# Performance work log

Hardware: AMD Instinct MI355X
Metric: run time of the kernel (lower is better)

## Reference

```python
import jax, jax.numpy as jnp
import numpy as np
from jax import lax

D = 8          # conv_out_size
HID = 128      # lstm hidden
EMB = 32       # word embed
GD = 256       # g/f mlp width


def _coords():
    # faithful to cvt_coord with python3 float division on first component
    c = np.zeros((D * D, 2), dtype=np.float32)
    for i in range(D * D):
        c[i, 0] = (i / D - D / 2) / (D / 2.0)
        c[i, 1] = (i % D - D / 2) / (D / 2.0)
    return jnp.asarray(c)


def _conv_bn(x, k, b, gamma, beta):
    y = lax.conv_general_dilated(x, k, (2, 2), [(1, 1), (1, 1)],
                                 dimension_numbers=('NCHW', 'OIHW', 'NCHW'))
    y = jax.nn.relu(y + b[None, :, None, None])
    m = y.mean((0, 2, 3))
    v = ((y - m[None, :, None, None]) ** 2).mean((0, 2, 3))  # biased var (train-mode BN)
    y = (y - m[None, :, None, None]) * lax.rsqrt(v + 1e-5)[None, :, None, None]
    return gamma[None, :, None, None] * y + beta[None, :, None, None]


def setup_inputs() -> dict:
    key = jax.random.key(0)
    ks = iter(jax.random.split(key, 48))
    B, T, QV, AV = 64, 18, 90, 28
    n = lambda sh, s=0.1: jax.random.normal(next(ks), sh, jnp.float32) * s
    inp = {
        'img': jax.random.normal(next(ks), (B, 3, 128, 128), jnp.float32),
        'qst_idxs': jax.random.randint(next(ks), (B, T), 0, QV),
        'emb': n((QV, EMB)).at[0].set(0.0),  # padding_idx=0
        'W_ih': n((4 * HID, EMB)), 'W_hh': n((4 * HID, HID)),
        'b_ih': n((4 * HID,)), 'b_hh': n((4 * HID,)),
        'k1': n((24, 3, 3, 3)), 'cb1': n((24,)), 'g1': jnp.ones((24,)), 'be1': jnp.zeros((24,)),
        'k2': n((24, 24, 3, 3)), 'cb2': n((24,)), 'g2': jnp.ones((24,)), 'be2': jnp.zeros((24,)),
        'k3': n((24, 24, 3, 3)), 'cb3': n((24,)), 'g3': jnp.ones((24,)), 'be3': jnp.zeros((24,)),
        'k4': n((24, 24, 3, 3)), 'cb4': n((24,)), 'g4': jnp.ones((24,)), 'be4': jnp.zeros((24,)),
        'Wg1': n((GD, 180)), 'bg1': n((GD,)),
        'Wg2': n((GD, GD)), 'bg2': n((GD,)),
        'Wg3': n((GD, GD)), 'bg3': n((GD,)),
        'Wg4': n((GD, GD)), 'bg4': n((GD,)),
        'Wf1': n((GD, GD)), 'bf1': n((GD,)),
        'Wf2': n((GD, GD)), 'bf2': n((GD,)),
        'Wf3': n((AV, GD)), 'bf3': n((AV,)),
        'h0': jax.random.normal(next(ks), (B, HID), jnp.float32),
        'c0': jax.random.normal(next(ks), (B, HID), jnp.float32),
    }
    return inp


def reference(img, qst_idxs, emb, W_ih, W_hh, b_ih, b_hh,
              k1, cb1, g1, be1, k2, cb2, g2, be2, k3, cb3, g3, be3, k4, cb4, g4, be4,
              Wg1, bg1, Wg2, bg2, Wg3, bg3, Wg4, bg4,
              Wf1, bf1, Wf2, bf2, Wf3, bf3, h0, c0):
    B = img.shape[0]
    # --- question encoder: embedding (padding_idx=0) + LSTM, take final CELL state ---
    we = emb[qst_idxs] * (qst_idxs != 0)[..., None].astype(emb.dtype)  # [B,T,32]

    def step(carry, x_t):
        h, c = carry
        gates = x_t @ W_ih.T + h @ W_hh.T + (b_ih + b_hh)
        i, f, g, o = jnp.split(gates, 4, axis=-1)
        c = jax.nn.sigmoid(f) * c + jax.nn.sigmoid(i) * jnp.tanh(g)
        h = jax.nn.sigmoid(o) * jnp.tanh(c)
        return (h, c), None

    (h_n, c_n), _ = lax.scan(step, (h0, c0), we.transpose(1, 0, 2))
    qst = c_n  # original uses self.hidden[1][-1] == cell state, [B,128]

    # --- conv stack ---
    x = _conv_bn(img, k1, cb1, g1, be1)
    x = _conv_bn(x, k2, cb2, g2, be2)
    x = _conv_bn(x, k3, cb3, g3, be3)
    x = _conv_bn(x, k4, cb4, g4, be4)  # [B,24,8,8]

    xf = x.reshape(B, 24, D * D).transpose(0, 2, 1)            # [B,64,24]
    xf = jnp.concatenate([xf, jnp.broadcast_to(_coords(), (B, D * D, 2))], 2)  # [B,64,26]

    # --- g-MLP over all pairs; first linear decomposed across x_i / x_j / qst ---
    # pair (k,j) feature = [x_flat[j](26), x_flat[k](26), qst(128)]
    Ai = xf @ Wg1[:, :26].T                    # [B,64,256], x_i part (index j)
    Aj = xf @ Wg1[:, 26:52].T                  # [B,64,256], x_j part (index k)
    Q = qst @ Wg1[:, 52:].T + bg1              # [B,256]
    h = jax.nn.relu(Ai[:, None, :, :] + Aj[:, :, None, :] + Q[:, None, None, :])  # [B,64,64,256]
    h = jax.nn.relu(h @ Wg2.T + bg2)
    h = jax.nn.relu(h @ Wg3.T + bg3)
    h = jax.nn.relu(h @ Wg4.T + bg4)
    xg = h.sum((1, 2))                          # [B,256] sum-pool over pairs

    # --- f-MLP (dropout = identity in eval) ---
    xfc = jax.nn.relu(xg @ Wf1.T + bf1)
    xfc = jax.nn.relu(xfc @ Wf2.T + bf2)
    logits = xfc @ Wf3.T + bf3
    return jax.nn.log_softmax(logits, axis=-1)
```

## Files before the change

kernel.cpp:

```cpp
#include <hip/hip_runtime.h>
#include <math.h>

typedef __bf16 bf16x8 __attribute__((ext_vector_type(8)));
typedef float  f32x16 __attribute__((ext_vector_type(16)));

#define DEVFN __device__ __forceinline__

DEVFN unsigned short f2bfh(float f) {
    __bf16 h = (__bf16)f;
    union { __bf16 h; unsigned short u; } v; v.h = h;
    return v.u;
}
DEVFN float sigmoidf_(float x) { return 1.0f / (1.0f + expf(-x)); }

__global__ void cvt_kernel(const float* __restrict__ Wg2, const float* __restrict__ Wg3,
                           const float* __restrict__ Wg4,
                           const float* __restrict__ Wih, const float* __restrict__ Whh,
                           unsigned short* __restrict__ Wt2, unsigned short* __restrict__ Wt3,
                           unsigned short* __restrict__ Wt4,
                           float* __restrict__ WihT, float* __restrict__ WhhT)
{
    int i = blockIdx.x * 512 + threadIdx.x;
    if (i < 196608) {
        int seg = i >> 16, idx = i & 65535;
        const float* src = (seg == 0) ? Wg2 : (seg == 1) ? Wg3 : Wg4;
        unsigned short* dst = (seg == 0) ? Wt2 : (seg == 1) ? Wt3 : Wt4;
        int col = idx >> 8, k = idx & 255;
        dst[(k >> 3)*2048 + col*8 + (k & 7)] = f2bfh(src[idx]);
    } else {
        int j = i - 196608;
        if (j < 65536) {
            int d = j >> 9, row = j & 511;
            WhhT[j] = Whh[row*128 + d];
        } else if (j < 81920) {
            j -= 65536;
            int d = j >> 9, row = j & 511;
            WihT[j] = Wih[row*32 + d];
        }
    }
}

__global__ void lstm_kernel(const int* __restrict__ qidx, const float* __restrict__ emb,
                            const float* __restrict__ WihT, const float* __restrict__ WhhT,
                            const float* __restrict__ bih, const float* __restrict__ bhh,
                            const float* __restrict__ h0, const float* __restrict__ c0,
                            float* __restrict__ qst)
{
    int b = blockIdx.x, tid = threadIdx.x;
    __shared__ float hs[128], cs[128], xs[32], gs[512];
    if (tid < 128) { hs[tid] = h0[b*128 + tid]; cs[tid] = c0[b*128 + tid]; }
    float bsum = bih[tid] + bhh[tid];
    for (int t = 0; t < 18; ++t) {
        if (tid < 32) {
            int id = qidx[b*18 + t];
            xs[tid] = (id != 0) ? emb[id*32 + tid] : 0.0f;
        }
        __syncthreads();
        float g = bsum;
        #pragma unroll
        for (int d = 0; d < 32; ++d) g += xs[d] * WihT[d*512 + tid];
        #pragma unroll 8
        for (int d = 0; d < 128; ++d) g += hs[d] * WhhT[d*512 + tid];
        gs[tid] = g;
        __syncthreads();
        if (tid < 128) {
            float ig = sigmoidf_(gs[tid]);
            float fg = sigmoidf_(gs[128 + tid]);
            float gg = tanhf(gs[256 + tid]);
            float og = sigmoidf_(gs[384 + tid]);
            float cn = fg * cs[tid] + ig * gg;
            cs[tid] = cn;
            hs[tid] = og * tanhf(cn);
        }
        __syncthreads();
    }
    if (tid < 128) qst[b*128 + tid] = cs[tid];
}

__launch_bounds__(256, 4)
__global__ void conv1_kernel(const float* __restrict__ img, const float* __restrict__ wk,
                             const float* __restrict__ cb, float* __restrict__ y1)
{
    __shared__ float simg[3][9][128];
    __shared__ __align__(16) float wl[3][9][24];
    __shared__ float cbs[24];
    int b = blockIdx.x, t = blockIdx.y, tid = threadIdx.x;
    for (int i = tid; i < 648; i += 256) {
        int co = i / 27, rem = i % 27;
        wl[rem / 9][rem % 9][co] = wk[i];
    }
    if (tid < 24) cbs[tid] = cb[tid];
    int base = 8*t - 1;
    for (int i = tid; i < 3*9*128; i += 256) {
        int ci = i / (9*128); int r2 = i % (9*128);
        int row = r2 / 128, colx = r2 % 128;
        int ih = base + row;
        simg[ci][row][colx] = (ih >= 0 && ih < 128) ?
            img[((size_t)(b*3 + ci)*128 + ih)*128 + colx] : 0.f;
    }
    __syncthreads();

    int ow = tid & 63;
    int os = tid >> 6;
    int oh = t*4 + os;
    float* yb = y1 + ((size_t)b*24*64 + oh)*64 + ow;

    #pragma unroll
    for (int co4 = 0; co4 < 24; co4 += 4) {
        float a0 = 0.f, a1 = 0.f, a2 = 0.f, a3 = 0.f;
        #pragma unroll
        for (int ci = 0; ci < 3; ++ci)
          #pragma unroll
          for (int kh = 0; kh < 3; ++kh)
            #pragma unroll
            for (int kw = 0; kw < 3; ++kw) {
                int iw = ow*2 + kw - 1;
                float x = (iw >= 0 && iw < 128) ? simg[ci][2*os + kh][iw] : 0.f;
                float4 w4 = *reinterpret_cast<const float4*>(&wl[ci][kh*3 + kw][co4]);
                a0 += x*w4.x; a1 += x*w4.y; a2 += x*w4.z; a3 += x*w4.w;
            }
        yb[(size_t)(co4+0)*4096] = fmaxf(a0 + cbs[co4+0], 0.f);
        yb[(size_t)(co4+1)*4096] = fmaxf(a1 + cbs[co4+1], 0.f);
        yb[(size_t)(co4+2)*4096] = fmaxf(a2 + cbs[co4+2], 0.f);
        yb[(size_t)(co4+3)*4096] = fmaxf(a3 + cbs[co4+3], 0.f);
    }
}

__global__ void bn_partial_kernel(const float* __restrict__ y, float* __restrict__ part,
                                  int HW, int nb)
{
    int c = blockIdx.x;
    int s = blockIdx.y;
    int S = gridDim.y;
    int tid = threadIdx.x;
    int n4 = HW >> 2;
    float sum = 0.f, sum2 = 0.f;
    for (int b = s * nb; b < (s + 1) * nb; ++b) {
        const float4* p = reinterpret_cast<const float4*>(y + ((size_t)(b*24 + c)) * HW);
        for (int i = tid; i < n4; i += 256) {
            float4 v = p[i];
            sum  += v.x + v.y + v.z + v.w;
            sum2 += v.x*v.x + v.y*v.y + v.z*v.z + v.w*v.w;
        }
    }
    __shared__ float rs[256], rs2[256];
    rs[tid] = sum; rs2[tid] = sum2;
    __syncthreads();
    for (int st = 128; st > 0; st >>= 1) {
        if (tid < st) { rs[tid] += rs[tid + st]; rs2[tid] += rs2[tid + st]; }
        __syncthreads();
    }
    if (tid == 0) {
        part[(c * S + s) * 2]     = rs[0];
        part[(c * S + s) * 2 + 1] = rs2[0];
    }
}

#define BN_FOLD(bnp, gamma, beta, S, N, abs_, abo_, tid)                    \
    if (tid < 24) {                                                          \
        float s_ = 0.f, s2_ = 0.f;                                           \
        for (int i_ = 0; i_ < (S); ++i_) {                                   \
            s_  += (bnp)[((tid)*(S) + i_)*2];                                \
            s2_ += (bnp)[((tid)*(S) + i_)*2 + 1];                            \
        }                                                                    \
        float m_ = s_ / (N);                                                 \
        float v_ = s2_ / (N) - m_*m_;                                        \
        float r_ = rsqrtf(v_ + 1e-5f);                                       \
        float a_ = (gamma)[tid] * r_;                                        \
        (abs_)[tid] = a_; (abo_)[tid] = (beta)[tid] - m_*a_;                 \
    }

__launch_bounds__(128, 4)
__global__ void conv2_kernel(const float* __restrict__ y1, const float* __restrict__ wk,
                             const float* __restrict__ cb,
                             const float* __restrict__ bnp, const float* __restrict__ gamma,
                             const float* __restrict__ beta,
                             float* __restrict__ y2)
{
    __shared__ float sin2[24][5][64];
    __shared__ float wl[24][9][24];
    __shared__ float cbs[24];
    __shared__ float abs_[24], abo_[24];
    int b = blockIdx.x, t = blockIdx.y, tid = threadIdx.x;
    BN_FOLD(bnp, gamma, beta, 16, 262144, abs_, abo_, tid);
    for (int i = tid; i < 5184; i += 128) {
        int co = i / 216, rem = i % 216;
        int ci = rem / 9, tap = rem % 9;
        wl[ci][tap][co] = wk[i];
    }
    if (tid < 24) cbs[tid] = cb[tid];
    __syncthreads();
    int base = 4*t - 1;
    for (int i = tid; i < 24*5*64; i += 128) {
        int ci = i / (5*64); int r2 = i % (5*64);
        int row = r2 / 64, colx = r2 % 64;
        int ih = base + row;
        sin2[ci][row][colx] = (ih >= 0 && ih < 64) ?
            y1[((size_t)(b*24 + ci)*64 + ih)*64 + colx] * abs_[ci] + abo_[ci] : 0.f;
    }
    __syncthreads();

    int pos = tid & 63;
    int ow = pos & 31, os = pos >> 5;
    int ch = tid >> 6;
    int oh = 2*t + os;
    float acc[12];
    #pragma unroll
    for (int c = 0; c < 12; ++c) acc[c] = 0.f;

    for (int ci = 0; ci < 24; ++ci) {
        #pragma unroll
        for (int kh = 0; kh < 3; ++kh)
          #pragma unroll
          for (int kw = 0; kw < 3; ++kw) {
            int iw = ow*2 + kw - 1;
            float x = (iw >= 0 && iw < 64) ? sin2[ci][2*os + kh][iw] : 0.f;
            const float* wv = &wl[ci][kh*3 + kw][ch*12];
            #pragma unroll
            for (int c4 = 0; c4 < 3; ++c4) {
                float4 w4 = *reinterpret_cast<const float4*>(wv + c4*4);
                acc[c4*4+0] += x*w4.x;
                acc[c4*4+1] += x*w4.y;
                acc[c4*4+2] += x*w4.z;
                acc[c4*4+3] += x*w4.w;
            }
          }
    }
    #pragma unroll
    for (int c = 0; c < 12; ++c) {
        int co = ch*12 + c;
        y2[((size_t)(b*24 + co)*32 + oh)*32 + ow] = fmaxf(acc[c] + cbs[co], 0.f);
    }
}

__launch_bounds__(256, 2)
__global__ void conv_kernel(const float* __restrict__ in, const float* __restrict__ wk,
                            const float* __restrict__ cb,
                            const float* __restrict__ bnp, const float* __restrict__ gamma,
                            const float* __restrict__ beta, int S, int N,
                            float* __restrict__ out,
                            int Cin, int Hin, int Win, int Hout, int Wout)
{
    int cob = blockIdx.x;
    int co = cob % 24, b = cob / 24;
    int tid = threadIdx.x;
    __shared__ float sw[24*9];
    __shared__ float so9[9];
    __shared__ float bias;
    __shared__ float abs_[24], abo_[24];
    BN_FOLD(bnp, gamma, beta, S, N, abs_, abo_, tid);
    __syncthreads();
    if (tid < Cin*9) {
        int ci = tid / 9, t = tid % 9;
        sw[tid] = wk[(co*Cin + ci)*9 + t] * abs_[ci];
    }
    if (tid < 9) {
        float s = 0.f;
        for (int ci = 0; ci < Cin; ++ci)
            s += abo_[ci] * wk[(co*Cin + ci)*9 + tid];
        so9[tid] = s;
    }
    if (tid == 0) bias = cb[co];
    __syncthreads();

    int HW = Hout * Wout;
    int pos = tid;
    if (pos >= HW) return;
    int ow = pos % Wout, oh = pos / Wout;

    float acc = bias;
    #pragma unroll
    for (int kh = 0; kh < 3; ++kh) {
        int ih = oh*2 + kh - 1;
        bool vh = (ih >= 0 && ih < Hin);
        #pragma unroll
        for (int kw = 0; kw < 3; ++kw) {
            int iw = ow*2 + kw - 1;
            if (vh && iw >= 0 && iw < Win) acc += so9[kh*3 + kw];
        }
    }
    const float* ipb = in + ((size_t)b * Cin) * Hin * Win;
    for (int ci = 0; ci < Cin; ++ci) {
        const float* ip = ipb + (size_t)ci * Hin * Win;
        const float* swp = sw + ci*9;
        #pragma unroll
        for (int kh = 0; kh < 3; ++kh) {
            int ih = oh*2 + kh - 1;
            if (ih < 0 || ih >= Hin) continue;
            #pragma unroll
            for (int kw = 0; kw < 3; ++kw) {
                int iw = ow*2 + kw - 1;
                if (iw < 0 || iw >= Win) continue;
                acc += ip[ih*Win + iw] * swp[kh*3 + kw];
            }
        }
    }
    out[((size_t)(b*24 + co)) * HW + pos] = fmaxf(acc, 0.0f);
}

__global__ void aiajq_kernel(const float* __restrict__ y4,
                             const float* __restrict__ bnp, const float* __restrict__ gamma,
                             const float* __restrict__ beta,
                             const float* __restrict__ qst,
                             const float* __restrict__ Wg1, const float* __restrict__ bg1,
                             float* __restrict__ Ai, float* __restrict__ Aj, float* __restrict__ Q)
{
    int b = blockIdx.x, c = threadIdx.x;
    __shared__ float xfl[64 * 26];
    __shared__ float qv[128];
    __shared__ float abs_[24], abo_[24];
    BN_FOLD(bnp, gamma, beta, 1, 4096, abs_, abo_, c);
    __syncthreads();
    for (int i = c; i < 64*24; i += 256) {
        int p = i / 24, ch = i % 24;
        xfl[p*26 + ch] = y4[((size_t)(b*24 + ch)) * 64 + p] * abs_[ch] + abo_[ch];
    }
    if (c < 64) {
        xfl[c*26 + 24] = ((float)c / 8.0f - 4.0f) * 0.25f;
        xfl[c*26 + 25] = ((float)(c % 8) - 4.0f) * 0.25f;
    }
    if (c < 128) qv[c] = qst[b*128 + c];
    __syncthreads();
    const float* w = Wg1 + (size_t)c * 180;
    float wa[26], wb[26];
    #pragma unroll
    for (int d = 0; d < 26; ++d) { wa[d] = w[d]; wb[d] = w[26 + d]; }
    float q = bg1[c];
    for (int d = 0; d < 128; ++d) q += qv[d] * w[52 + d];
    Q[b*256 + c] = q;
    for (int j = 0; j < 64; ++j) {
        const float* xr = xfl + j*26;
        float sa = 0.f, sb = 0.f;
        #pragma unroll
        for (int d = 0; d < 26; ++d) { sa += xr[d]*wa[d]; sb += xr[d]*wb[d]; }
        Ai[((size_t)(b*64 + j))*256 + c] = sa;
        Aj[((size_t)(b*64 + j))*256 + c] = sb;
    }
}

__launch_bounds__(512, 4)
__global__ void gmlp_kernel(const float* __restrict__ Ai, const float* __restrict__ Aj,
                            const float* __restrict__ Q,
                            const unsigned short* __restrict__ Wt2, const float* __restrict__ bg2,
                            const unsigned short* __restrict__ Wt3, const float* __restrict__ bg3,
                            const unsigned short* __restrict__ Wt4, const float* __restrict__ bg4,
                            float* __restrict__ partial)
{
    constexpr int LDP = 264;
    __shared__ __align__(16) unsigned short buf[128 * LDP];
    int tid = threadIdx.x;
    int blk = blockIdx.x;
    int b = blk >> 5;
    int k0 = (blk & 31) << 1;

    {
        int g  = tid >> 8;
        int jh = (tid >> 7) & 1;
        int c2 = tid & 127;
        float2 aj = *((const float2*)(Aj + ((size_t)(b*64 + k0 + g))*256) + c2);
        float2 qq = *((const float2*)(Q + b*256) + c2);
        float a0 = aj.x + qq.x, a1 = aj.y + qq.y;
        const float2* aip = (const float2*)(Ai + ((size_t)b*64)*256) + c2;
        #pragma unroll 4
        for (int j = jh*32; j < jh*32 + 32; ++j) {
            float2 av = aip[(size_t)j*128];
            unsigned lo = f2bfh(fmaxf(av.x + a0, 0.f));
            unsigned hv = f2bfh(fmaxf(av.y + a1, 0.f));
            *(unsigned*)(&buf[(size_t)(g*64 + j)*LDP + 2*c2]) = lo | (hv << 16);
        }
    }
    __syncthreads();

    int l = tid & 63, w = tid >> 6;
    int rh = w >> 2;
    int cg = w & 3;
    int lid = l & 31, hi = l >> 5;
    int arow = rh*64 + lid;
    int colA = cg*64 + lid;
    int colB = colA + 32;

    const unsigned short* Ws[3] = {Wt2, Wt3, Wt4};
    const float* Bs[3] = {bg2, bg3, bg4};

    #pragma unroll
    for (int layer = 0; layer < 3; ++layer) {
        const unsigned short* W = Ws[layer];
        const float* bias = Bs[layer];
        f32x16 acc00, acc01, acc10, acc11;
        #pragma unroll
        for (int i = 0; i < 16; ++i) { acc00[i]=0.f; acc01[i]=0.f; acc10[i]=0.f; acc11[i]=0.f; }

        const unsigned short* wp0 = W + (size_t)hi*2048 + colA*8;
        const unsigned short* wp1 = W + (size_t)hi*2048 + colB*8;
        const unsigned short* ap  = buf + arow*LDP + hi*8;

        #pragma unroll
        for (int kk = 0; kk < 16; ++kk) {
            bf16x8 b0 = *reinterpret_cast<const bf16x8*>(wp0 + kk*4096);
            bf16x8 b1 = *reinterpret_cast<const bf16x8*>(wp1 + kk*4096);
            bf16x8 a0 = *reinterpret_cast<const bf16x8*>(ap + kk*16);
            bf16x8 a1 = *reinterpret_cast<const bf16x8*>(ap + 32*LDP + kk*16);
            acc00 = __builtin_amdgcn_mfma_f32_32x32x16_bf16(a0, b0, acc00, 0, 0, 0);
            acc01 = __builtin_amdgcn_mfma_f32_32x32x16_bf16(a0, b1, acc01, 0, 0, 0);
            acc10 = __builtin_amdgcn_mfma_f32_32x32x16_bf16(a1, b0, acc10, 0, 0, 0);
            acc11 = __builtin_amdgcn_mfma_f32_32x32x16_bf16(a1, b1, acc11, 0, 0, 0);
        }

        if (layer < 2) {
            float bc0 = bias[colA], bc1 = bias[colB];
            __syncthreads();
            #pragma unroll
            for (int reg = 0; reg < 16; ++reg) {
                int r0 = rh*64 + (reg & 3) + 8*(reg >> 2) + 4*hi;
                buf[r0*LDP + colA] = f2bfh(fmaxf(acc00[reg] + bc0, 0.f));
                buf[r0*LDP + colB] = f2bfh(fmaxf(acc01[reg] + bc1, 0.f));
                int r1 = r0 + 32;
                buf[r1*LDP + colA] = f2bfh(fmaxf(acc10[reg] + bc0, 0.f));
                buf[r1*LDP + colB] = f2bfh(fmaxf(acc11[reg] + bc1, 0.f));
            }
            __syncthreads();
        } else {
            float bc0 = bias[colA], bc1 = bias[colB];
            float cs0 = 0.f, cs1 = 0.f;
            #pragma unroll
            for (int reg = 0; reg < 16; ++reg) {
                cs0 += fmaxf(acc00[reg] + bc0, 0.f) + fmaxf(acc10[reg] + bc0, 0.f);
                cs1 += fmaxf(acc01[reg] + bc1, 0.f) + fmaxf(acc11[reg] + bc1, 0.f);
            }
            cs0 += __shfl_xor(cs0, 32);
            cs1 += __shfl_xor(cs1, 32);
            if (hi == 0) {
                float* pp = partial + ((size_t)blk*2 + rh)*256;
                pp[colA] = cs0;
                pp[colB] = cs1;
            }
        }
    }
}

__global__ void fmlp_kernel(const float* __restrict__ partial,
                            const float* __restrict__ Wf1, const float* __restrict__ bf1,
                            const float* __restrict__ Wf2, const float* __restrict__ bf2,
                            const float* __restrict__ Wf3, const float* __restrict__ bf3,
                            float* __restrict__ out)
{
    int b = blockIdx.x, tid = threadIdx.x;
    __shared__ float v0[256], v1[256], lgt[28];
    {
        float s0 = 0.f, s1 = 0.f, s2 = 0.f, s3 = 0.f;
        const float* p = partial + ((size_t)b * 64) * 256 + tid;
        #pragma unroll
        for (int k = 0; k < 64; k += 4) {
            s0 += p[(size_t)(k+0) * 256];
            s1 += p[(size_t)(k+1) * 256];
            s2 += p[(size_t)(k+2) * 256];
            s3 += p[(size_t)(k+3) * 256];
        }
        v0[tid] = (s0 + s1) + (s2 + s3);
    }
    __syncthreads();
    {
        float s = bf1[tid];
        const float4* wr = reinterpret_cast<const float4*>(Wf1 + (size_t)tid * 256);
        for (int k4 = 0; k4 < 64; ++k4) {
            float4 wv = wr[k4];
            s += wv.x*v0[k4*4+0] + wv.y*v0[k4*4+1] + wv.z*v0[k4*4+2] + wv.w*v0[k4*4+3];
        }
        v1[tid] = fmaxf(s, 0.f);
    }
    __syncthreads();
    {
        float s = bf2[tid];
        const float4* wr = reinterpret_cast<const float4*>(Wf2 + (size_t)tid * 256);
        for (int k4 = 0; k4 < 64; ++k4) {
            float4 wv = wr[k4];
            s += wv.x*v1[k4*4+0] + wv.y*v1[k4*4+1] + wv.z*v1[k4*4+2] + wv.w*v1[k4*4+3];
        }
        v0[tid] = fmaxf(s, 0.f);
    }
    __syncthreads();
    if (tid < 28) {
        float s = bf3[tid];
        const float4* wr = reinterpret_cast<const float4*>(Wf3 + (size_t)tid * 256);
        for (int k4 = 0; k4 < 64; ++k4) {
            float4 wv = wr[k4];
            s += wv.x*v0[k4*4+0] + wv.y*v0[k4*4+1] + wv.z*v0[k4*4+2] + wv.w*v0[k4*4+3];
        }
        lgt[tid] = s;
    }
    __syncthreads();
    if (tid == 0) {
        float mx = -1e30f;
        for (int i = 0; i < 28; ++i) mx = fmaxf(mx, lgt[i]);
        float se = 0.f;
        for (int i = 0; i < 28; ++i) se += expf(lgt[i] - mx);
        float lse = mx + logf(se);
        for (int i = 0; i < 28; ++i) out[b*28 + i] = lgt[i] - lse;
    }
}

extern "C" void kernel_launch(void* const* d_in, const int* in_sizes, int n_in,
                              void* d_out, int out_size, void* d_ws, size_t ws_size,
                              hipStream_t stream)
{
    (void)in_sizes; (void)n_in; (void)out_size; (void)ws_size;
    const float* img = (const float*)d_in[0];
    const int*   qidx= (const int*)  d_in[1];
    const float* emb = (const float*)d_in[2];
    const float* Wih = (const float*)d_in[3];
    const float* Whh = (const float*)d_in[4];
    const float* bih = (const float*)d_in[5];
    const float* bhh = (const float*)d_in[6];
    const float* k1  = (const float*)d_in[7];  const float* cb1=(const float*)d_in[8];
    const float* g1  = (const float*)d_in[9];  const float* be1=(const float*)d_in[10];
    const float* k2  = (const float*)d_in[11]; const float* cb2=(const float*)d_in[12];
    const float* g2  = (const float*)d_in[13]; const float* be2=(const float*)d_in[14];
    const float* k3  = (const float*)d_in[15]; const float* cb3=(const float*)d_in[16];
    const float* g3  = (const float*)d_in[17]; const float* be3=(const float*)d_in[18];
    const float* k4  = (const float*)d_in[19]; const float* cb4=(const float*)d_in[20];
    const float* g4  = (const float*)d_in[21]; const float* be4=(const float*)d_in[22];
    const float* Wg1 = (const float*)d_in[23]; const float* bg1=(const float*)d_in[24];
    const float* Wg2 = (const float*)d_in[25]; const float* bg2=(const float*)d_in[26];
    const float* Wg3 = (const float*)d_in[27]; const float* bg3=(const float*)d_in[28];
    const float* Wg4 = (const float*)d_in[29]; const float* bg4=(const float*)d_in[30];
    const float* Wf1 = (const float*)d_in[31]; const float* bf1=(const float*)d_in[32];
    const float* Wf2 = (const float*)d_in[33]; const float* bf2=(const float*)d_in[34];
    const float* Wf3 = (const float*)d_in[35]; const float* bf3=(const float*)d_in[36];
    const float* h0  = (const float*)d_in[37]; const float* c0 =(const float*)d_in[38];
    float* out = (float*)d_out;

    float* ws = (float*)d_ws;
    float* y1 = ws;   ws += 64*24*64*64;
    float* y2 = ws;   ws += 64*24*32*32;
    float* y3 = ws;   ws += 64*24*16*16;
    float* y4 = ws;   ws += 64*24*8*8;
    float* bnp = ws;  ws += 24*16*2;
    float* qst = ws;  ws += 64*128;
    float* Ai  = ws;  ws += 64*64*256;
    float* Aj  = ws;  ws += 64*64*256;
    float* Qb  = ws;  ws += 64*256;
    unsigned short* Wt2 = (unsigned short*)ws; ws += 65536/2;
    unsigned short* Wt3 = (unsigned short*)ws; ws += 65536/2;
    unsigned short* Wt4 = (unsigned short*)ws; ws += 65536/2;
    float* WihT = ws; ws += 32*512;
    float* WhhT = ws; ws += 128*512;
    float* partial = ws; ws += 2048*2*256;

    cvt_kernel<<<544, 512, 0, stream>>>(Wg2, Wg3, Wg4, Wih, Whh, Wt2, Wt3, Wt4, WihT, WhhT);
    lstm_kernel<<<64, 512, 0, stream>>>(qidx, emb, WihT, WhhT, bih, bhh, h0, c0, qst);

    conv1_kernel<<<dim3(64, 16), 256, 0, stream>>>(img, k1, cb1, y1);
    bn_partial_kernel<<<dim3(24,16), 256, 0, stream>>>(y1, bnp, 64*64, 4);
    conv2_kernel<<<dim3(64, 16), 128, 0, stream>>>(y1, k2, cb2, bnp, g1, be1, y2);
    bn_partial_kernel<<<dim3(24,8), 256, 0, stream>>>(y2, bnp, 32*32, 8);
    conv_kernel<<<dim3(64*24, 1), 256, 0, stream>>>(y2, k3, cb3, bnp, g2, be2, 8, 64*32*32,
                                                    y3, 24, 32, 32, 16, 16);
    bn_partial_kernel<<<dim3(24,4), 256, 0, stream>>>(y3, bnp, 16*16, 16);
    conv_kernel<<<dim3(64*24, 1), 256, 0, stream>>>(y3, k4, cb4, bnp, g3, be3, 4, 64*16*16,
                                                    y4, 24, 16, 16, 8, 8);
    bn_partial_kernel<<<dim3(24,1), 256, 0, stream>>>(y4, bnp, 8*8, 64);

    aiajq_kernel<<<64, 256, 0, stream>>>(y4, bnp, g4, be4, qst, Wg1, bg1, Ai, Aj, Qb);

    gmlp_kernel<<<2048, 512, 0, stream>>>(Ai, Aj, Qb, Wt2, bg2, Wt3, bg3, Wt4, bg4, partial);
    fmlp_kernel<<<64, 256, 0, stream>>>(partial, Wf1, bf1, Wf2, bf2, Wf3, bf3, out);
}
```

Baseline: 456.9 us.

## Fuse BN statistics into conv epilogues via atomics and merge weight prep with conv1

```diff
diff --git a/kernel.cpp b/kernel.cpp
--- a/kernel.cpp
+++ b/kernel.cpp
@@ -13,30 +13,122 @@
 }
 DEVFN float sigmoidf_(float x) { return 1.0f / (1.0f + expf(-x)); }
 
-__global__ void cvt_kernel(const float* __restrict__ Wg2, const float* __restrict__ Wg3,
-                           const float* __restrict__ Wg4,
-                           const float* __restrict__ Wih, const float* __restrict__ Whh,
-                           unsigned short* __restrict__ Wt2, unsigned short* __restrict__ Wt3,
-                           unsigned short* __restrict__ Wt4,
-                           float* __restrict__ WihT, float* __restrict__ WhhT)
-{
-    int i = blockIdx.x * 512 + threadIdx.x;
-    if (i < 196608) {
-        int seg = i >> 16, idx = i & 65535;
-        const float* src = (seg == 0) ? Wg2 : (seg == 1) ? Wg3 : Wg4;
-        unsigned short* dst = (seg == 0) ? Wt2 : (seg == 1) ? Wt3 : Wt4;
-        int col = idx >> 8, k = idx & 255;
-        dst[(k >> 3)*2048 + col*8 + (k & 7)] = f2bfh(src[idx]);
-    } else {
-        int j = i - 196608;
-        if (j < 65536) {
-            int d = j >> 9, row = j & 511;
-            WhhT[j] = Whh[row*128 + d];
-        } else if (j < 81920) {
-            j -= 65536;
-            int d = j >> 9, row = j & 511;
-            WihT[j] = Wih[row*32 + d];
-        }
+#define BN_FOLD1(bnp, gamma, beta, N, abs_, abo_, tid)                      \
+    if (tid < 24) {                                                          \
+        float s_  = (bnp)[(tid)*2];                                          \
+        float s2_ = (bnp)[(tid)*2 + 1];                                      \
+        float m_ = s_ / (N);                                                 \
+        float v_ = s2_ / (N) - m_*m_;                                        \
+        float r_ = rsqrtf(v_ + 1e-5f);                                       \
+        float a_ = (gamma)[tid] * r_;                                        \
+        (abs_)[tid] = a_; (abo_)[tid] = (beta)[tid] - m_*a_;                 \
+    }
+
+DEVFN float wsum(float v) {
+    #pragma unroll
+    for (int off = 32; off > 0; off >>= 1) v += __shfl_down(v, off);
+    return v;
+}
+
+__launch_bounds__(256, 4)
+__global__ void prep_conv1_kernel(const float* __restrict__ img, const float* __restrict__ wk,
+                                  const float* __restrict__ cb, float* __restrict__ y1,
+                                  float* __restrict__ bnp1,
+                                  const float* __restrict__ Wg2, const float* __restrict__ Wg3,
+                                  const float* __restrict__ Wg4,
+                                  const float* __restrict__ Wih, const float* __restrict__ Whh,
+                                  unsigned short* __restrict__ Wt2, unsigned short* __restrict__ Wt3,
+                                  unsigned short* __restrict__ Wt4,
+                                  float* __restrict__ WihT, float* __restrict__ WhhT)
+{
+    int blk = blockIdx.x, tid = threadIdx.x;
+    if (blk >= 1024) {
+        int i = (blk - 1024) * 256 + tid;
+        if (i < 196608) {
+            int seg = i >> 16, idx = i & 65535;
+            const float* src = (seg == 0) ? Wg2 : (seg == 1) ? Wg3 : Wg4;
+            unsigned short* dst = (seg == 0) ? Wt2 : (seg == 1) ? Wt3 : Wt4;
+            int col = idx >> 8, k = idx & 255;
+            dst[(k >> 3)*2048 + col*8 + (k & 7)] = f2bfh(src[idx]);
+        } else {
+            int j = i - 196608;
+            if (j < 65536) {
+                int d = j >> 9, row = j & 511;
+                WhhT[j] = Whh[row*128 + d];
+            } else {
+                j -= 65536;
+                int d = j >> 9, row = j & 511;
+                WihT[j] = Wih[row*32 + d];
+            }
+        }
+        return;
+    }
+    __shared__ float simg[3][9][128];
+    __shared__ __align__(16) float wl[3][9][24];
+    __shared__ float cbs[24];
+    __shared__ float bs[4][24], bs2[4][24];
+    int b = blk >> 4, t = blk & 15;
+    for (int i = tid; i < 648; i += 256) {
+        int co = i / 27, rem = i % 27;
+        wl[rem / 9][rem % 9][co] = wk[i];
+    }
+    if (tid < 24) cbs[tid] = cb[tid];
+    for (int i = tid; i < 96; i += 256) { bs[i / 24][i % 24] = 0.f; bs2[i / 24][i % 24] = 0.f; }
+    int base = 8*t - 1;
+    for (int i = tid; i < 3*9*128; i += 256) {
+        int ci = i / (9*128); int r2 = i % (9*128);
+        int row = r2 / 128, colx = r2 % 128;
+        int ih = base + row;
+        simg[ci][row][colx] = (ih >= 0 && ih < 128) ?
+            img[((size_t)(b*3 + ci)*128 + ih)*128 + colx] : 0.f;
+    }
+    __syncthreads();
+
+    int ow = tid & 63;
+    int os = tid >> 6;
+    int oh = t*4 + os;
+    int wv = tid >> 6, ln = tid & 63;
+    float* yb = y1 + ((size_t)b*24*64 + oh)*64 + ow;
+
+    #pragma unroll
+    for (int co4 = 0; co4 < 24; co4 += 4) {
+        float a0 = 0.f, a1 = 0.f, a2 = 0.f, a3 = 0.f;
+        #pragma unroll
+        for (int ci = 0; ci < 3; ++ci)
+          #pragma unroll
+          for (int kh = 0; kh < 3; ++kh)
+            #pragma unroll
+            for (int kw = 0; kw < 3; ++kw) {
+                int iw = ow*2 + kw - 1;
+                float x = (iw >= 0 && iw < 128) ? simg[ci][2*os + kh][iw] : 0.f;
+                float4 w4 = *reinterpret_cast<const float4*>(&wl[ci][kh*3 + kw][co4]);
+                a0 += x*w4.x; a1 += x*w4.y; a2 += x*w4.z; a3 += x*w4.w;
+            }
+        float v0 = fmaxf(a0 + cbs[co4+0], 0.f);
+        float v1 = fmaxf(a1 + cbs[co4+1], 0.f);
+        float v2 = fmaxf(a2 + cbs[co4+2], 0.f);
+        float v3 = fmaxf(a3 + cbs[co4+3], 0.f);
+        yb[(size_t)(co4+0)*4096] = v0;
+        yb[(size_t)(co4+1)*4096] = v1;
+        yb[(size_t)(co4+2)*4096] = v2;
+        yb[(size_t)(co4+3)*4096] = v3;
+        float s0 = wsum(v0), q0 = wsum(v0*v0);
+        float s1 = wsum(v1), q1 = wsum(v1*v1);
+        float s2 = wsum(v2), q2 = wsum(v2*v2);
+        float s3 = wsum(v3), q3 = wsum(v3*v3);
+        if (ln == 0) {
+            bs[wv][co4+0] += s0; bs2[wv][co4+0] += q0;
+            bs[wv][co4+1] += s1; bs2[wv][co4+1] += q1;
+            bs[wv][co4+2] += s2; bs2[wv][co4+2] += q2;
+            bs[wv][co4+3] += s3; bs2[wv][co4+3] += q3;
+        }
+    }
+    __syncthreads();
+    if (tid < 24) {
+        float S  = bs[0][tid] + bs[1][tid] + bs[2][tid] + bs[3][tid];
+        float S2 = bs2[0][tid] + bs2[1][tid] + bs2[2][tid] + bs2[3][tid];
+        atomicAdd(&bnp1[tid*2], S);
+        atomicAdd(&bnp1[tid*2 + 1], S2);
     }
 }
 
@@ -77,112 +169,20 @@
     if (tid < 128) qst[b*128 + tid] = cs[tid];
 }
 
-__launch_bounds__(256, 4)
-__global__ void conv1_kernel(const float* __restrict__ img, const float* __restrict__ wk,
-                             const float* __restrict__ cb, float* __restrict__ y1)
-{
-    __shared__ float simg[3][9][128];
-    __shared__ __align__(16) float wl[3][9][24];
-    __shared__ float cbs[24];
-    int b = blockIdx.x, t = blockIdx.y, tid = threadIdx.x;
-    for (int i = tid; i < 648; i += 256) {
-        int co = i / 27, rem = i % 27;
-        wl[rem / 9][rem % 9][co] = wk[i];
-    }
-    if (tid < 24) cbs[tid] = cb[tid];
-    int base = 8*t - 1;
-    for (int i = tid; i < 3*9*128; i += 256) {
-        int ci = i / (9*128); int r2 = i % (9*128);
-        int row = r2 / 128, colx = r2 % 128;
-        int ih = base + row;
-        simg[ci][row][colx] = (ih >= 0 && ih < 128) ?
-            img[((size_t)(b*3 + ci)*128 + ih)*128 + colx] : 0.f;
-    }
-    __syncthreads();
-
-    int ow = tid & 63;
-    int os = tid >> 6;
-    int oh = t*4 + os;
-    float* yb = y1 + ((size_t)b*24*64 + oh)*64 + ow;
-
-    #pragma unroll
-    for (int co4 = 0; co4 < 24; co4 += 4) {
-        float a0 = 0.f, a1 = 0.f, a2 = 0.f, a3 = 0.f;
-        #pragma unroll
-        for (int ci = 0; ci < 3; ++ci)
-          #pragma unroll
-          for (int kh = 0; kh < 3; ++kh)
-            #pragma unroll
-            for (int kw = 0; kw < 3; ++kw) {
-                int iw = ow*2 + kw - 1;
-                float x = (iw >= 0 && iw < 128) ? simg[ci][2*os + kh][iw] : 0.f;
-                float4 w4 = *reinterpret_cast<const float4*>(&wl[ci][kh*3 + kw][co4]);
-                a0 += x*w4.x; a1 += x*w4.y; a2 += x*w4.z; a3 += x*w4.w;
-            }
-        yb[(size_t)(co4+0)*4096] = fmaxf(a0 + cbs[co4+0], 0.f);
-        yb[(size_t)(co4+1)*4096] = fmaxf(a1 + cbs[co4+1], 0.f);
-        yb[(size_t)(co4+2)*4096] = fmaxf(a2 + cbs[co4+2], 0.f);
-        yb[(size_t)(co4+3)*4096] = fmaxf(a3 + cbs[co4+3], 0.f);
-    }
-}
-
-__global__ void bn_partial_kernel(const float* __restrict__ y, float* __restrict__ part,
-                                  int HW, int nb)
-{
-    int c = blockIdx.x;
-    int s = blockIdx.y;
-    int S = gridDim.y;
-    int tid = threadIdx.x;
-    int n4 = HW >> 2;
-    float sum = 0.f, sum2 = 0.f;
-    for (int b = s * nb; b < (s + 1) * nb; ++b) {
-        const float4* p = reinterpret_cast<const float4*>(y + ((size_t)(b*24 + c)) * HW);
-        for (int i = tid; i < n4; i += 256) {
-            float4 v = p[i];
-            sum  += v.x + v.y + v.z + v.w;
-            sum2 += v.x*v.x + v.y*v.y + v.z*v.z + v.w*v.w;
-        }
-    }
-    __shared__ float rs[256], rs2[256];
-    rs[tid] = sum; rs2[tid] = sum2;
-    __syncthreads();
-    for (int st = 128; st > 0; st >>= 1) {
-        if (tid < st) { rs[tid] += rs[tid + st]; rs2[tid] += rs2[tid + st]; }
-        __syncthreads();
-    }
-    if (tid == 0) {
-        part[(c * S + s) * 2]     = rs[0];
-        part[(c * S + s) * 2 + 1] = rs2[0];
-    }
-}
-
-#define BN_FOLD(bnp, gamma, beta, S, N, abs_, abo_, tid)                    \
-    if (tid < 24) {                                                          \
-        float s_ = 0.f, s2_ = 0.f;                                           \
-        for (int i_ = 0; i_ < (S); ++i_) {                                   \
-            s_  += (bnp)[((tid)*(S) + i_)*2];                                \
-            s2_ += (bnp)[((tid)*(S) + i_)*2 + 1];                            \
-        }                                                                    \
-        float m_ = s_ / (N);                                                 \
-        float v_ = s2_ / (N) - m_*m_;                                        \
-        float r_ = rsqrtf(v_ + 1e-5f);                                       \
-        float a_ = (gamma)[tid] * r_;                                        \
-        (abs_)[tid] = a_; (abo_)[tid] = (beta)[tid] - m_*a_;                 \
-    }
-
 __launch_bounds__(128, 4)
 __global__ void conv2_kernel(const float* __restrict__ y1, const float* __restrict__ wk,
                              const float* __restrict__ cb,
                              const float* __restrict__ bnp, const float* __restrict__ gamma,
                              const float* __restrict__ beta,
-                             float* __restrict__ y2)
+                             float* __restrict__ y2, float* __restrict__ bnp2)
 {
     __shared__ float sin2[24][5][64];
     __shared__ float wl[24][9][24];
     __shared__ float cbs[24];
     __shared__ float abs_[24], abo_[24];
+    __shared__ float bss[24], bss2[24];
     int b = blockIdx.x, t = blockIdx.y, tid = threadIdx.x;
-    BN_FOLD(bnp, gamma, beta, 16, 262144, abs_, abo_, tid);
+    BN_FOLD1(bnp, gamma, beta, 262144.f, abs_, abo_, tid);
     for (int i = tid; i < 5184; i += 128) {
         int co = i / 216, rem = i % 216;
         int ci = rem / 9, tap = rem % 9;
@@ -203,6 +203,7 @@
     int pos = tid & 63;
     int ow = pos & 31, os = pos >> 5;
     int ch = tid >> 6;
+    int ln = tid & 63;
     int oh = 2*t + os;
     float acc[12];
     #pragma unroll
@@ -229,7 +230,15 @@
     #pragma unroll
     for (int c = 0; c < 12; ++c) {
         int co = ch*12 + c;
-        y2[((size_t)(b*24 + co)*32 + oh)*32 + ow] = fmaxf(acc[c] + cbs[co], 0.f);
+        float v = fmaxf(acc[c] + cbs[co], 0.f);
+        y2[((size_t)(b*24 + co)*32 + oh)*32 + ow] = v;
+        float s = wsum(v), q = wsum(v*v);
+        if (ln == 0) { bss[co] = s; bss2[co] = q; }
+    }
+    __syncthreads();
+    if (tid < 24) {
+        atomicAdd(&bnp2[tid*2], bss[tid]);
+        atomicAdd(&bnp2[tid*2 + 1], bss2[tid]);
     }
 }
 
@@ -237,8 +246,8 @@
 __global__ void conv_kernel(const float* __restrict__ in, const float* __restrict__ wk,
                             const float* __restrict__ cb,
                             const float* __restrict__ bnp, const float* __restrict__ gamma,
-                            const float* __restrict__ beta, int S, int N,
-                            float* __restrict__ out,
+                            const float* __restrict__ beta, float Nprev,
+                            float* __restrict__ out, float* __restrict__ bnp_out,
                             int Cin, int Hin, int Win, int Hout, int Wout)
 {
     int cob = blockIdx.x;
@@ -248,7 +257,8 @@
     __shared__ float so9[9];
     __shared__ float bias;
     __shared__ float abs_[24], abo_[24];
-    BN_FOLD(bnp, gamma, beta, S, N, abs_, abo_, tid);
+    __shared__ float rs[256], rs2[256];
+    BN_FOLD1(bnp, gamma, beta, Nprev, abs_, abo_, tid);
     __syncthreads();
     if (tid < Cin*9) {
         int ci = tid / 9, t = tid % 9;
@@ -265,37 +275,49 @@
 
     int HW = Hout * Wout;
     int pos = tid;
-    if (pos >= HW) return;
-    int ow = pos % Wout, oh = pos / Wout;
-
-    float acc = bias;
-    #pragma unroll
-    for (int kh = 0; kh < 3; ++kh) {
-        int ih = oh*2 + kh - 1;
-        bool vh = (ih >= 0 && ih < Hin);
-        #pragma unroll
-        for (int kw = 0; kw < 3; ++kw) {
-            int iw = ow*2 + kw - 1;
-            if (vh && iw >= 0 && iw < Win) acc += so9[kh*3 + kw];
-        }
-    }
-    const float* ipb = in + ((size_t)b * Cin) * Hin * Win;
-    for (int ci = 0; ci < Cin; ++ci) {
-        const float* ip = ipb + (size_t)ci * Hin * Win;
-        const float* swp = sw + ci*9;
+    float v = 0.f;
+    if (pos < HW) {
+        int ow = pos % Wout, oh = pos / Wout;
+        float acc = bias;
         #pragma unroll
         for (int kh = 0; kh < 3; ++kh) {
             int ih = oh*2 + kh - 1;
-            if (ih < 0 || ih >= Hin) continue;
+            bool vh = (ih >= 0 && ih < Hin);
             #pragma unroll
             for (int kw = 0; kw < 3; ++kw) {
                 int iw = ow*2 + kw - 1;
-                if (iw < 0 || iw >= Win) continue;
-                acc += ip[ih*Win + iw] * swp[kh*3 + kw];
-            }
-        }
-    }
-    out[((size_t)(b*24 + co)) * HW + pos] = fmaxf(acc, 0.0f);
+                if (vh && iw >= 0 && iw < Win) acc += so9[kh*3 + kw];
+            }
+        }
+        const float* ipb = in + ((size_t)b * Cin) * Hin * Win;
+        for (int ci = 0; ci < Cin; ++ci) {
+            const float* ip = ipb + (size_t)ci * Hin * Win;
+            const float* swp = sw + ci*9;
+            #pragma unroll
+            for (int kh = 0; kh < 3; ++kh) {
+                int ih = oh*2 + kh - 1;
+                if (ih < 0 || ih >= Hin) continue;
+                #pragma unroll
+                for (int kw = 0; kw < 3; ++kw) {
+                    int iw = ow*2 + kw - 1;
+                    if (iw < 0 || iw >= Win) continue;
+                    acc += ip[ih*Win + iw] * swp[kh*3 + kw];
+                }
+            }
+        }
+        v = fmaxf(acc, 0.0f);
+        out[((size_t)(b*24 + co)) * HW + pos] = v;
+    }
+    rs[tid] = v; rs2[tid] = v*v;
+    __syncthreads();
+    for (int st = 128; st > 0; st >>= 1) {
+        if (tid < st) { rs[tid] += rs[tid + st]; rs2[tid] += rs2[tid + st]; }
+        __syncthreads();
+    }
+    if (tid == 0) {
+        atomicAdd(&bnp_out[co*2], rs[0]);
+        atomicAdd(&bnp_out[co*2 + 1], rs2[0]);
+    }
 }
 
 __global__ void aiajq_kernel(const float* __restrict__ y4,
@@ -309,7 +331,7 @@
     __shared__ float xfl[64 * 26];
     __shared__ float qv[128];
     __shared__ float abs_[24], abo_[24];
-    BN_FOLD(bnp, gamma, beta, 1, 4096, abs_, abo_, c);
+    BN_FOLD1(bnp, gamma, beta, 4096.f, abs_, abo_, c);
     __syncthreads();
     for (int i = c; i < 64*24; i += 256) {
         int p = i / 24, ch = i % 24;
@@ -394,12 +416,19 @@
         const unsigned short* wp1 = W + (size_t)hi*2048 + colB*8;
         const unsigned short* ap  = buf + arow*LDP + hi*8;
 
+        bf16x8 nb0 = *reinterpret_cast<const bf16x8*>(wp0);
+        bf16x8 nb1 = *reinterpret_cast<const bf16x8*>(wp1);
+        bf16x8 na0 = *reinterpret_cast<const bf16x8*>(ap);
+        bf16x8 na1 = *reinterpret_cast<const bf16x8*>(ap + 32*LDP);
         #pragma unroll
         for (int kk = 0; kk < 16; ++kk) {
-            bf16x8 b0 = *reinterpret_cast<const bf16x8*>(wp0 + kk*4096);
-            bf16x8 b1 = *reinterpret_cast<const bf16x8*>(wp1 + kk*4096);
-            bf16x8 a0 = *reinterpret_cast<const bf16x8*>(ap + kk*16);
-            bf16x8 a1 = *reinterpret_cast<const bf16x8*>(ap + 32*LDP + kk*16);
+            bf16x8 b0 = nb0, b1 = nb1, a0 = na0, a1 = na1;
+            if (kk < 15) {
+                nb0 = *reinterpret_cast<const bf16x8*>(wp0 + (kk+1)*4096);
+                nb1 = *reinterpret_cast<const bf16x8*>(wp1 + (kk+1)*4096);
+                na0 = *reinterpret_cast<const bf16x8*>(ap + (kk+1)*16);
+                na1 = *reinterpret_cast<const bf16x8*>(ap + 32*LDP + (kk+1)*16);
+            }
             acc00 = __builtin_amdgcn_mfma_f32_32x32x16_bf16(a0, b0, acc00, 0, 0, 0);
             acc01 = __builtin_amdgcn_mfma_f32_32x32x16_bf16(a0, b1, acc01, 0, 0, 0);
             acc10 = __builtin_amdgcn_mfma_f32_32x32x16_bf16(a1, b0, acc10, 0, 0, 0);
@@ -534,7 +563,8 @@
     float* y2 = ws;   ws += 64*24*32*32;
     float* y3 = ws;   ws += 64*24*16*16;
     float* y4 = ws;   ws += 64*24*8*8;
-    float* bnp = ws;  ws += 24*16*2;
+    float* bnp = ws;  ws += 192;
+    float* bnp1 = bnp, *bnp2 = bnp + 48, *bnp3 = bnp + 96, *bnp4 = bnp + 144;
     float* qst = ws;  ws += 64*128;
     float* Ai  = ws;  ws += 64*64*256;
     float* Aj  = ws;  ws += 64*64*256;
@@ -546,21 +576,20 @@
     float* WhhT = ws; ws += 128*512;
     float* partial = ws; ws += 2048*2*256;
 
-    cvt_kernel<<<544, 512, 0, stream>>>(Wg2, Wg3, Wg4, Wih, Whh, Wt2, Wt3, Wt4, WihT, WhhT);
+    hipMemsetAsync(bnp, 0, 192*sizeof(float), stream);
+
+    prep_conv1_kernel<<<2112, 256, 0, stream>>>(img, k1, cb1, y1, bnp1,
+                                                Wg2, Wg3, Wg4, Wih, Whh,
+                                                Wt2, Wt3, Wt4, WihT, WhhT);
     lstm_kernel<<<64, 512, 0, stream>>>(qidx, emb, WihT, WhhT, bih, bhh, h0, c0, qst);
 
-    conv1_kernel<<<dim3(64, 16), 256, 0, stream>>>(img, k1, cb1, y1);
-    bn_partial_kernel<<<dim3(24,16), 256, 0, stream>>>(y1, bnp, 64*64, 4);
-    conv2_kernel<<<dim3(64, 16), 128, 0, stream>>>(y1, k2, cb2, bnp, g1, be1, y2);
-    bn_partial_kernel<<<dim3(24,8), 256, 0, stream>>>(y2, bnp, 32*32, 8);
-    conv_kernel<<<dim3(64*24, 1), 256, 0, stream>>>(y2, k3, cb3, bnp, g2, be2, 8, 64*32*32,
-                                                    y3, 24, 32, 32, 16, 16);
-    bn_partial_kernel<<<dim3(24,4), 256, 0, stream>>>(y3, bnp, 16*16, 16);
-    conv_kernel<<<dim3(64*24, 1), 256, 0, stream>>>(y3, k4, cb4, bnp, g3, be3, 4, 64*16*16,
-                                                    y4, 24, 16, 16, 8, 8);
-    bn_partial_kernel<<<dim3(24,1), 256, 0, stream>>>(y4, bnp, 8*8, 64);
-
-    aiajq_kernel<<<64, 256, 0, stream>>>(y4, bnp, g4, be4, qst, Wg1, bg1, Ai, Aj, Qb);
+    conv2_kernel<<<dim3(64, 16), 128, 0, stream>>>(y1, k2, cb2, bnp1, g1, be1, y2, bnp2);
+    conv_kernel<<<1536, 256, 0, stream>>>(y2, k3, cb3, bnp2, g2, be2, 65536.f,
+                                          y3, bnp3, 24, 32, 32, 16, 16);
+    conv_kernel<<<1536, 256, 0, stream>>>(y3, k4, cb4, bnp3, g3, be3, 16384.f,
+                                          y4, bnp4, 24, 16, 16, 8, 8);
+
+    aiajq_kernel<<<64, 256, 0, stream>>>(y4, bnp4, g4, be4, qst, Wg1, bg1, Ai, Aj, Qb);
 
     gmlp_kernel<<<2048, 512, 0, stream>>>(Ai, Aj, Qb, Wt2, bg2, Wt3, bg3, Wt4, bg4, partial);
     fmlp_kernel<<<64, 256, 0, stream>>>(partial, Wf1, bf1, Wf2, bf2, Wf3, bf3, out);
```

Measured after the change: 505.3 us. 1.11x slower.
